# Kernel tuning notes

Measured on AMD Instinct MI355X. Metric: run time of the kernel, lower is better.

The kernel has to match this reference:

```python
import jax, jax.numpy as jnp
import numpy as np

L1 = 256
INPUTS = 41024
FACTOR_INPUTS = 64
B = 2048


def setup_inputs() -> dict:
    key = jax.random.key(0)
    k_us, k_them, k_w, k_b, k_W, k_bias = jax.random.split(key, 6)
    us = jax.random.uniform(k_us, (B, 1), dtype=jnp.float32)
    them = jax.random.uniform(k_them, (B, 1), dtype=jnp.float32)
    w_in = jax.random.uniform(k_w, (B, INPUTS), dtype=jnp.float32)
    b_in = jax.random.uniform(k_b, (B, INPUTS), dtype=jnp.float32)
    # Linear weight [L1, INPUTS]; last FACTOR_INPUTS columns zeroed as in __init__
    W = jax.random.normal(k_W, (L1, INPUTS), dtype=jnp.float32) * 0.01
    W = W.at[:, INPUTS - FACTOR_INPUTS:].set(0.0)
    bias = jax.random.normal(k_bias, (L1,), dtype=jnp.float32) * 0.01
    return {"us": us, "them": them, "w_in": w_in, "b_in": b_in, "W": W, "bias": bias}


def reference(us, them, w_in, b_in, W, bias):
    # sparse-feature linear (dense reference): [B, INPUTS] @ [INPUTS, L1]
    w = jnp.dot(w_in, W.T) + bias          # [B, L1]
    b = jnp.dot(b_in, W.T) + bias          # [B, L1]
    wb = jnp.concatenate([w, b], axis=1)   # [B, 2*L1]
    bw = jnp.concatenate([b, w], axis=1)   # [B, 2*L1]
    l0 = us * wb + them * bw               # perspective mix
    return jnp.clip(l0, 0.0, 1.0)          # Hardtanh(0, 1) == clipped relu
```

## Files before the change

kernel.cpp:

```cpp
#include <hip/hip_runtime.h>
#include <stdint.h>

#define C_INPUTS 41024
#define C_KEFF   40960
#define C_L1     256
#define C_BATCH  2048
#define C_BK     64
#define C_MTILE  64
#define C_KSPLIT 8
#define C_KCHUNK (C_KEFF / C_KSPLIT)
#define C_NITER  (C_KCHUNK / C_BK)
#define C_MBLOCKS (4096 / C_MTILE)
#define C_WTILE_BYTES (C_L1 * C_BK * 2)
#define C_NKTILES (C_KEFF / C_BK)
#define WS_W_BYTES ((size_t)C_L1 * C_KEFF * 2)
#define LDS_BUF_BYTES 40960
#define LDS_TOTAL (2 * LDS_BUF_BYTES)

typedef __attribute__((ext_vector_type(8))) short  short8;
typedef __attribute__((ext_vector_type(4))) short  short4v;
typedef __attribute__((ext_vector_type(4))) float  f32x4;

typedef __attribute__((address_space(1))) const uint32_t g_as1_u32;
typedef __attribute__((address_space(3))) uint32_t      l_as3_u32;

__device__ __forceinline__ uint16_t bf16_rtne(float f) {
  uint32_t u = __builtin_bit_cast(uint32_t, f);
  u += 0x7fffu + ((u >> 16) & 1u);
  return (uint16_t)(u >> 16);
}

__global__ __launch_bounds__(256) void k_convert_w(const float* __restrict__ W,
                                                   uint16_t* __restrict__ wsW) {
  const int kt = blockIdx.x;
  const int t  = threadIdx.x;
  const int g  = t & 7;
  const int r0 = t >> 3;
  const float* src = W + (size_t)kt * C_BK + (size_t)g * 8;
  uint16_t* dstT = wsW + (size_t)kt * (C_L1 * C_BK);
#pragma unroll
  for (int p = 0; p < 8; ++p) {
    const int row = p * 32 + r0;
    const float4* s = (const float4*)(src + (size_t)row * C_INPUTS);
    float4 x = s[0];
    float4 y = s[1];
    union { uint16_t h[8]; short8 v; } u;
    u.h[0] = bf16_rtne(x.x); u.h[1] = bf16_rtne(x.y);
    u.h[2] = bf16_rtne(x.z); u.h[3] = bf16_rtne(x.w);
    u.h[4] = bf16_rtne(y.x); u.h[5] = bf16_rtne(y.y);
    u.h[6] = bf16_rtne(y.z); u.h[7] = bf16_rtne(y.w);
    const int slot = g ^ (row & 7);
    *(short8*)(dstT + (size_t)row * C_BK + (slot << 3)) = u.v;
  }
}

__global__ __launch_bounds__(256, 2) void k_gemm(const float* __restrict__ w_in,
                                                 const float* __restrict__ b_in,
                                                 const uint16_t* __restrict__ wsW,
                                                 float* __restrict__ wsP) {
  extern __shared__ char smem[];
  const int bid  = blockIdx.x;
  const int ks   = bid & 7;
  const int mb   = bid >> 3;
  const int tid  = threadIdx.x;
  const int wave = tid >> 6;
  const int lane = tid & 63;

  const int k0 = ks * C_KCHUNK;
  const float* Abase = (mb < 32)
      ? (w_in + (size_t)mb * C_MTILE * C_INPUTS)
      : (b_in + (size_t)(mb - 32) * C_MTILE * C_INPUTS);

  const int ar = tid >> 2;
  const int ac = tid & 3;
  const float* aptr = Abase + (size_t)ar * C_INPUTS + k0 + ac * 4;

  const char* wg = (const char*)wsW + (size_t)(ks * C_NITER) * C_WTILE_BYTES + (size_t)tid * 16;

  const int lrow = lane & 15;
  const int lg   = lane >> 4;
  int aoff[4][2], boff[4][2];
#pragma unroll
  for (int mi = 0; mi < 4; ++mi)
#pragma unroll
    for (int kk = 0; kk < 2; ++kk) {
      const int r = mi * 16 + lrow;
      aoff[mi][kk] = r * 128 + (((kk * 4 + lg) ^ (r & 7)) << 4);
    }
#pragma unroll
  for (int ni = 0; ni < 4; ++ni)
#pragma unroll
    for (int kk = 0; kk < 2; ++kk) {
      const int r = wave * 64 + ni * 16 + lrow;
      boff[ni][kk] = 8192 + r * 128 + (((kk * 4 + lg) ^ (r & 7)) << 4);
    }

  int awoff[4];
#pragma unroll
  for (int s = 0; s < 4; ++s) {
    const int gg = s * 2 + (ac >> 1);
    awoff[s] = ar * 128 + (((gg) ^ (ar & 7)) << 4) + ((ac & 1) << 3);
  }

  f32x4 acc[4][4];
#pragma unroll
  for (int i = 0; i < 4; ++i)
#pragma unroll
    for (int j = 0; j < 4; ++j) acc[i][j] = (f32x4){0.f, 0.f, 0.f, 0.f};

  float4 av[4];

  {
    const float4* p = (const float4*)aptr;
#pragma unroll
    for (int s = 0; s < 4; ++s) av[s] = p[s * 4];
#pragma unroll
    for (int c = 0; c < 8; ++c) {
      __builtin_amdgcn_global_load_lds((g_as1_u32*)(wg + c * 4096),
                                       (l_as3_u32*)(smem + 8192 + wave * 1024 + c * 4096),
                                       16, 0, 0);
    }
    char* ab = smem;
#pragma unroll
    for (int s = 0; s < 4; ++s) {
      union { uint16_t h[4]; short4v v; } u;
      u.h[0] = bf16_rtne(av[s].x); u.h[1] = bf16_rtne(av[s].y);
      u.h[2] = bf16_rtne(av[s].z); u.h[3] = bf16_rtne(av[s].w);
      *(short4v*)(ab + awoff[s]) = u.v;
    }
  }
  __syncthreads();

  int cur = 0;
#pragma unroll 1
  for (int it = 0; it < C_NITER; ++it) {
    const int nxt = cur ^ 1;
    const bool pf = (it + 1 < C_NITER);
    if (pf) {
      const float4* p = (const float4*)(aptr + (size_t)(it + 1) * C_BK);
#pragma unroll
      for (int s = 0; s < 4; ++s) av[s] = p[s * 4];
      const char* wsrc = wg + (size_t)(it + 1) * C_WTILE_BYTES;
      char* wdst = smem + nxt * LDS_BUF_BYTES + 8192 + wave * 1024;
#pragma unroll
      for (int c = 0; c < 8; ++c) {
        __builtin_amdgcn_global_load_lds((g_as1_u32*)(wsrc + c * 4096),
                                         (l_as3_u32*)(wdst + c * 4096),
                                         16, 0, 0);
      }
    }

    {
      const char* ab = smem + cur * LDS_BUF_BYTES;
#pragma unroll
      for (int kk = 0; kk < 2; ++kk) {
        short8 af[4], bf[4];
#pragma unroll
        for (int mi = 0; mi < 4; ++mi) af[mi] = *(const short8*)(ab + aoff[mi][kk]);
#pragma unroll
        for (int ni = 0; ni < 4; ++ni) bf[ni] = *(const short8*)(ab + boff[ni][kk]);
#pragma unroll
        for (int mi = 0; mi < 4; ++mi)
#pragma unroll
          for (int ni = 0; ni < 4; ++ni)
            acc[mi][ni] = __builtin_amdgcn_mfma_f32_16x16x32_bf16(af[mi], bf[ni], acc[mi][ni], 0, 0, 0);
      }
    }

    if (pf) {
      char* ab = smem + nxt * LDS_BUF_BYTES;
#pragma unroll
      for (int s = 0; s < 4; ++s) {
        union { uint16_t h[4]; short4v v; } u;
        u.h[0] = bf16_rtne(av[s].x); u.h[1] = bf16_rtne(av[s].y);
        u.h[2] = bf16_rtne(av[s].z); u.h[3] = bf16_rtne(av[s].w);
        *(short4v*)(ab + awoff[s]) = u.v;
      }
    }
    __syncthreads();
    cur = nxt;
  }

  float* P = wsP + ((size_t)ks * 4096 + (size_t)mb * C_MTILE) * 256;
#pragma unroll
  for (int mi = 0; mi < 4; ++mi)
#pragma unroll
    for (int ni = 0; ni < 4; ++ni)
#pragma unroll
      for (int j = 0; j < 4; ++j) {
        const int rr = mi * 16 + lg * 4 + j;
        const int cc = wave * 64 + ni * 16 + lrow;
        P[(size_t)rr * 256 + cc] = acc[mi][ni][j];
      }
}

__global__ __launch_bounds__(256) void k_reduce(const float* __restrict__ wsP,
                                                const float* __restrict__ us,
                                                const float* __restrict__ them,
                                                const float* __restrict__ bias,
                                                float* __restrict__ out) {
  const int r = blockIdx.x;
  const int c = threadIdx.x;
  float wd = 0.f, bd = 0.f;
#pragma unroll
  for (int s = 0; s < C_KSPLIT; ++s) {
    wd += wsP[((size_t)s * 4096 + r) * 256 + c];
    bd += wsP[((size_t)s * 4096 + 2048 + r) * 256 + c];
  }
  const float bi = bias[c];
  const float w = wd + bi;
  const float b = bd + bi;
  const float u = us[r];
  const float t = them[r];
  float o1 = u * w + t * b;
  float o2 = u * b + t * w;
  o1 = fminf(fmaxf(o1, 0.f), 1.f);
  o2 = fminf(fmaxf(o2, 0.f), 1.f);
  out[(size_t)r * 512 + c]       = o1;
  out[(size_t)r * 512 + 256 + c] = o2;
}

extern "C" void kernel_launch(void* const* d_in, const int* in_sizes, int n_in,
                              void* d_out, int out_size, void* d_ws, size_t ws_size,
                              hipStream_t stream) {
  const float* us   = (const float*)d_in[0];
  const float* them = (const float*)d_in[1];
  const float* w_in = (const float*)d_in[2];
  const float* b_in = (const float*)d_in[3];
  const float* W    = (const float*)d_in[4];
  const float* bias = (const float*)d_in[5];
  float* out = (float*)d_out;

  uint16_t* wsW = (uint16_t*)d_ws;
  float*    wsP = (float*)((char*)d_ws + WS_W_BYTES);

  k_convert_w<<<C_NKTILES, 256, 0, stream>>>(W, wsW);
  k_gemm<<<C_MBLOCKS * C_KSPLIT, 256, LDS_TOTAL, stream>>>(w_in, b_in, wsW, wsP);
  k_reduce<<<C_BATCH, 256, 0, stream>>>(wsP, us, them, bias, out);
}
```

Measured before the change: 211.7 us.

## Triple-buffer GEMM pipeline with BK=32 and MFMA-fragment-ordered LDS layout

Halves the K tile to 32 and moves from double to triple buffering in LDS, prefetching two tiles ahead. The loop is unrolled by two, with register ping-pong for the A activations and explicit vmcnt waits in place of full drains. The weight and activation tiles are stored in LDS already in MFMA fragment order, so each lane reads contiguous 16 bytes without XOR swizzle address math. The aim is better overlap of global loads with MFMA, paid for with twice as many barriers per K and reliance on hand-counted waitcnt values.

```diff
diff --git a/kernel.cpp b/kernel.cpp
--- a/kernel.cpp
+++ b/kernel.cpp
@@ -5,20 +5,21 @@
 #define C_KEFF   40960
 #define C_L1     256
 #define C_BATCH  2048
-#define C_BK     64
+#define C_BK     32
 #define C_MTILE  64
 #define C_KSPLIT 8
 #define C_KCHUNK (C_KEFF / C_KSPLIT)
 #define C_NITER  (C_KCHUNK / C_BK)
-#define C_MBLOCKS (4096 / C_MTILE)
-#define C_WTILE_BYTES (C_L1 * C_BK * 2)
-#define C_NKTILES (C_KEFF / C_BK)
+#define C_MBLOCKS 64
+#define C_NKT    (C_KEFF / C_BK)
+#define C_WTILE  (C_L1 * C_BK * 2)
+#define C_ATILE  (C_MTILE * C_BK * 2)
+#define C_BUF    (C_WTILE + C_ATILE)
+#define C_NBUF   3
+#define LDS_TOTAL (C_NBUF * C_BUF)
 #define WS_W_BYTES ((size_t)C_L1 * C_KEFF * 2)
-#define LDS_BUF_BYTES 40960
-#define LDS_TOTAL (2 * LDS_BUF_BYTES)
 
 typedef __attribute__((ext_vector_type(8))) short  short8;
-typedef __attribute__((ext_vector_type(4))) short  short4v;
 typedef __attribute__((ext_vector_type(4))) float  f32x4;
 
 typedef __attribute__((address_space(1))) const uint32_t g_as1_u32;
@@ -34,14 +35,17 @@
                                                    uint16_t* __restrict__ wsW) {
   const int kt = blockIdx.x;
   const int t  = threadIdx.x;
-  const int g  = t & 7;
-  const int r0 = t >> 3;
-  const float* src = W + (size_t)kt * C_BK + (size_t)g * 8;
-  uint16_t* dstT = wsW + (size_t)kt * (C_L1 * C_BK);
-#pragma unroll
-  for (int p = 0; p < 8; ++p) {
-    const int row = p * 32 + r0;
-    const float4* s = (const float4*)(src + (size_t)row * C_INPUTS);
+  const int l  = t & 63;
+  const int fb = t >> 6;
+  const int rm = l & 15;
+  const int kg = l >> 4;
+  const int kcol = kt * C_BK + kg * 8;
+  uint16_t* dst = wsW + (size_t)kt * (C_L1 * C_BK) + (size_t)l * 8;
+#pragma unroll
+  for (int q = 0; q < 4; ++q) {
+    const int f = fb * 4 + q;
+    const int row = f * 16 + rm;
+    const float4* s = (const float4*)(W + (size_t)row * C_INPUTS + kcol);
     float4 x = s[0];
     float4 y = s[1];
     union { uint16_t h[8]; short8 v; } u;
@@ -49,8 +53,7 @@
     u.h[2] = bf16_rtne(x.z); u.h[3] = bf16_rtne(x.w);
     u.h[4] = bf16_rtne(y.x); u.h[5] = bf16_rtne(y.y);
     u.h[6] = bf16_rtne(y.z); u.h[7] = bf16_rtne(y.w);
-    const int slot = g ^ (row & 7);
-    *(short8*)(dstT + (size_t)row * C_BK + (slot << 3)) = u.v;
+    *(short8*)(dst + (size_t)f * 512) = u.v;
   }
 }
 
@@ -65,6 +68,8 @@
   const int tid  = threadIdx.x;
   const int wave = tid >> 6;
   const int lane = tid & 63;
+  const int lrow = lane & 15;
+  const int lg   = lane >> 4;
 
   const int k0 = ks * C_KCHUNK;
   const float* Abase = (mb < 32)
@@ -73,113 +78,96 @@
 
   const int ar = tid >> 2;
   const int ac = tid & 3;
-  const float* aptr = Abase + (size_t)ar * C_INPUTS + k0 + ac * 4;
-
-  const char* wg = (const char*)wsW + (size_t)(ks * C_NITER) * C_WTILE_BYTES + (size_t)tid * 16;
-
-  const int lrow = lane & 15;
-  const int lg   = lane >> 4;
-  int aoff[4][2], boff[4][2];
-#pragma unroll
-  for (int mi = 0; mi < 4; ++mi)
-#pragma unroll
-    for (int kk = 0; kk < 2; ++kk) {
-      const int r = mi * 16 + lrow;
-      aoff[mi][kk] = r * 128 + (((kk * 4 + lg) ^ (r & 7)) << 4);
+  const float* aptr = Abase + (size_t)ar * C_INPUTS + k0 + ac * 8;
+  const int awoff = C_WTILE + ((ar >> 4) << 10) + ((ac * 16 + (ar & 15)) << 4);
+
+  const char* wg = (const char*)wsW + (size_t)(ks * C_NITER) * C_WTILE
+                 + (size_t)wave * 4096 + (size_t)lane * 16;
+
+  f32x4 acc[4][4];
+#pragma unroll
+  for (int i = 0; i < 4; ++i)
+#pragma unroll
+    for (int j = 0; j < 4; ++j) acc[i][j] = (f32x4){0.f, 0.f, 0.f, 0.f};
+
+  float4 avA[2], avB[2];
+  int cb = 0;
+
+  {
+#pragma unroll
+    for (int c = 0; c < 4; ++c) {
+      __builtin_amdgcn_global_load_lds((g_as1_u32*)(wg + c * 1024),
+                                       (l_as3_u32*)(smem + wave * 4096 + c * 1024), 16, 0, 0);
+      __builtin_amdgcn_global_load_lds((g_as1_u32*)(wg + C_WTILE + c * 1024),
+                                       (l_as3_u32*)(smem + C_BUF + wave * 4096 + c * 1024), 16, 0, 0);
     }
-#pragma unroll
-  for (int ni = 0; ni < 4; ++ni)
-#pragma unroll
-    for (int kk = 0; kk < 2; ++kk) {
-      const int r = wave * 64 + ni * 16 + lrow;
-      boff[ni][kk] = 8192 + r * 128 + (((kk * 4 + lg) ^ (r & 7)) << 4);
-    }
-
-  int awoff[4];
-#pragma unroll
-  for (int s = 0; s < 4; ++s) {
-    const int gg = s * 2 + (ac >> 1);
-    awoff[s] = ar * 128 + (((gg) ^ (ar & 7)) << 4) + ((ac & 1) << 3);
-  }
-
-  f32x4 acc[4][4];
-#pragma unroll
-  for (int i = 0; i < 4; ++i)
-#pragma unroll
-    for (int j = 0; j < 4; ++j) acc[i][j] = (f32x4){0.f, 0.f, 0.f, 0.f};
-
-  float4 av[4];
-
-  {
-    const float4* p = (const float4*)aptr;
-#pragma unroll
-    for (int s = 0; s < 4; ++s) av[s] = p[s * 4];
-#pragma unroll
-    for (int c = 0; c < 8; ++c) {
-      __builtin_amdgcn_global_load_lds((g_as1_u32*)(wg + c * 4096),
-                                       (l_as3_u32*)(smem + 8192 + wave * 1024 + c * 4096),
-                                       16, 0, 0);
-    }
-    char* ab = smem;
-#pragma unroll
-    for (int s = 0; s < 4; ++s) {
-      union { uint16_t h[4]; short4v v; } u;
-      u.h[0] = bf16_rtne(av[s].x); u.h[1] = bf16_rtne(av[s].y);
-      u.h[2] = bf16_rtne(av[s].z); u.h[3] = bf16_rtne(av[s].w);
-      *(short4v*)(ab + awoff[s]) = u.v;
-    }
-  }
-  __syncthreads();
-
-  int cur = 0;
+    const float4* p0 = (const float4*)aptr;
+    avA[0] = p0[0]; avA[1] = p0[1];
+    const float4* p1 = (const float4*)(aptr + C_BK);
+    avB[0] = p1[0]; avB[1] = p1[1];
+    union { uint16_t h[8]; short8 v; } u;
+    u.h[0] = bf16_rtne(avA[0].x); u.h[1] = bf16_rtne(avA[0].y);
+    u.h[2] = bf16_rtne(avA[0].z); u.h[3] = bf16_rtne(avA[0].w);
+    u.h[4] = bf16_rtne(avA[1].x); u.h[5] = bf16_rtne(avA[1].y);
+    u.h[6] = bf16_rtne(avA[1].z); u.h[7] = bf16_rtne(avA[1].w);
+    *(short8*)(smem + awoff) = u.v;
+    asm volatile("s_waitcnt vmcnt(0)" ::: "memory");
+    asm volatile("s_waitcnt lgkmcnt(0)" ::: "memory");
+    __builtin_amdgcn_s_barrier();
+    __builtin_amdgcn_sched_barrier(0);
+  }
+
+#define GEMM_STEP(T, AVI, AVC) do {                                          \
+    const bool pf = (T) + 2 < C_NITER;                                       \
+    const int nb1 = (cb + C_BUF < LDS_TOTAL) ? cb + C_BUF : cb + C_BUF - LDS_TOTAL; \
+    const int nb2 = (nb1 + C_BUF < LDS_TOTAL) ? nb1 + C_BUF : nb1 + C_BUF - LDS_TOTAL; \
+    if (pf) {                                                                \
+      const float4* p = (const float4*)(aptr + (size_t)((T) + 2) * C_BK);    \
+      AVI[0] = p[0]; AVI[1] = p[1];                                          \
+      const char* wsrc = wg + (size_t)((T) + 2) * C_WTILE;                   \
+      char* wdst = smem + nb2 + wave * 4096;                                 \
+      _Pragma("unroll")                                                      \
+      for (int c = 0; c < 4; ++c)                                            \
+        __builtin_amdgcn_global_load_lds((g_as1_u32*)(wsrc + c * 1024),      \
+                                         (l_as3_u32*)(wdst + c * 1024), 16, 0, 0); \
+    }                                                                        \
+    {                                                                        \
+      const char* ab = smem + cb;                                            \
+      short8 af[4], bf[4];                                                   \
+      _Pragma("unroll")                                                      \
+      for (int mi = 0; mi < 4; ++mi)                                         \
+        af[mi] = *(const short8*)(ab + C_WTILE + mi * 1024 + lane * 16);     \
+      _Pragma("unroll")                                                      \
+      for (int ni = 0; ni < 4; ++ni)                                         \
+        bf[ni] = *(const short8*)(ab + wave * 4096 + ni * 1024 + lane * 16); \
+      _Pragma("unroll")                                                      \
+      for (int mi = 0; mi < 4; ++mi)                                         \
+        _Pragma("unroll")                                                    \
+        for (int ni = 0; ni < 4; ++ni)                                       \
+          acc[mi][ni] = __builtin_amdgcn_mfma_f32_16x16x32_bf16(af[mi], bf[ni], acc[mi][ni], 0, 0, 0); \
+    }                                                                        \
+    if ((T) + 1 < C_NITER) {                                                 \
+      union { uint16_t h[8]; short8 v; } u;                                  \
+      u.h[0] = bf16_rtne(AVC[0].x); u.h[1] = bf16_rtne(AVC[0].y);            \
+      u.h[2] = bf16_rtne(AVC[0].z); u.h[3] = bf16_rtne(AVC[0].w);            \
+      u.h[4] = bf16_rtne(AVC[1].x); u.h[5] = bf16_rtne(AVC[1].y);            \
+      u.h[6] = bf16_rtne(AVC[1].z); u.h[7] = bf16_rtne(AVC[1].w);            \
+      *(short8*)(smem + nb1 + awoff) = u.v;                                  \
+    }                                                                        \
+    if (pf) { asm volatile("s_waitcnt vmcnt(6)" ::: "memory"); }             \
+    else    { asm volatile("s_waitcnt vmcnt(0)" ::: "memory"); }             \
+    asm volatile("s_waitcnt lgkmcnt(0)" ::: "memory");                       \
+    __builtin_amdgcn_s_barrier();                                            \
+    __builtin_amdgcn_sched_barrier(0);                                       \
+    cb = nb1;                                                                \
+  } while (0)
+
 #pragma unroll 1
-  for (int it = 0; it < C_NITER; ++it) {
-    const int nxt = cur ^ 1;
-    const bool pf = (it + 1 < C_NITER);
-    if (pf) {
-      const float4* p = (const float4*)(aptr + (size_t)(it + 1) * C_BK);
-#pragma unroll
-      for (int s = 0; s < 4; ++s) av[s] = p[s * 4];
-      const char* wsrc = wg + (size_t)(it + 1) * C_WTILE_BYTES;
-      char* wdst = smem + nxt * LDS_BUF_BYTES + 8192 + wave * 1024;
-#pragma unroll
-      for (int c = 0; c < 8; ++c) {
-        __builtin_amdgcn_global_load_lds((g_as1_u32*)(wsrc + c * 4096),
-                                         (l_as3_u32*)(wdst + c * 4096),
-                                         16, 0, 0);
-      }
-    }
-
-    {
-      const char* ab = smem + cur * LDS_BUF_BYTES;
-#pragma unroll
-      for (int kk = 0; kk < 2; ++kk) {
-        short8 af[4], bf[4];
-#pragma unroll
-        for (int mi = 0; mi < 4; ++mi) af[mi] = *(const short8*)(ab + aoff[mi][kk]);
-#pragma unroll
-        for (int ni = 0; ni < 4; ++ni) bf[ni] = *(const short8*)(ab + boff[ni][kk]);
-#pragma unroll
-        for (int mi = 0; mi < 4; ++mi)
-#pragma unroll
-          for (int ni = 0; ni < 4; ++ni)
-            acc[mi][ni] = __builtin_amdgcn_mfma_f32_16x16x32_bf16(af[mi], bf[ni], acc[mi][ni], 0, 0, 0);
-      }
-    }
-
-    if (pf) {
-      char* ab = smem + nxt * LDS_BUF_BYTES;
-#pragma unroll
-      for (int s = 0; s < 4; ++s) {
-        union { uint16_t h[4]; short4v v; } u;
-        u.h[0] = bf16_rtne(av[s].x); u.h[1] = bf16_rtne(av[s].y);
-        u.h[2] = bf16_rtne(av[s].z); u.h[3] = bf16_rtne(av[s].w);
-        *(short4v*)(ab + awoff[s]) = u.v;
-      }
-    }
-    __syncthreads();
-    cur = nxt;
-  }
+  for (int t = 0; t < C_NITER; t += 2) {
+    GEMM_STEP(t,     avA, avB);
+    GEMM_STEP(t + 1, avB, avA);
+  }
+#undef GEMM_STEP
 
   float* P = wsP + ((size_t)ks * 4096 + (size_t)mb * C_MTILE) * 256;
 #pragma unroll
@@ -234,7 +222,7 @@
   uint16_t* wsW = (uint16_t*)d_ws;
   float*    wsP = (float*)((char*)d_ws + WS_W_BYTES);
 
-  k_convert_w<<<C_NKTILES, 256, 0, stream>>>(W, wsW);
+  k_convert_w<<<C_NKT, 256, 0, stream>>>(W, wsW);
   k_gemm<<<C_MBLOCKS * C_KSPLIT, 256, LDS_TOTAL, stream>>>(w_in, b_in, wsW, wsP);
   k_reduce<<<C_BATCH, 256, 0, stream>>>(wsP, us, them, bias, out);
 }
```

Result: slower. 220.7 us (+4.3%).
